# Kernel optimization log

Measured on AMD Instinct MI355X. Metric: run time of the kernel, lower is better.

## Reference

```python
import jax, jax.numpy as jnp
import numpy as np

BETA_MIN = 0.01
BETA_MAX = 0.995
EPS = 1e-6


def setup_inputs() -> dict:
    key = jax.random.key(0)
    k1, k2, k3, k4 = jax.random.split(key, 4)
    B, T, D = 16, 4096, 128
    return {
        "q": jax.random.normal(k1, (B, T, D), dtype=jnp.float32),
        "k": jax.random.normal(k2, (B, T, D), dtype=jnp.float32),
        "v": jax.random.normal(k3, (B, T, D), dtype=jnp.float32),
        "beta": jax.random.uniform(k4, (B, T, 1), dtype=jnp.float32),
        "mask": jnp.ones((B, T, 1), dtype=jnp.float32),
        "base_beta_1": jnp.asarray(2.0, dtype=jnp.float32),
        "base_beta_2": jnp.asarray(3.0, dtype=jnp.float32),
    }


def _delta_scan(q, k, v, beta, mask, base_beta_1, base_beta_2):
    B, T, D = q.shape
    phi_q = jax.nn.elu(q) + 1.0  # positive feature map
    phi_k = jax.nn.elu(k) + 1.0
    b1_base = jnp.clip(jax.nn.sigmoid(base_beta_1), BETA_MIN, BETA_MAX)
    b2_base = jnp.clip(jax.nn.sigmoid(base_beta_2), BETA_MIN, BETA_MAX)

    # time-major for scan: [T, B, ...]
    xs = (
        jnp.swapaxes(phi_q, 0, 1),
        jnp.swapaxes(phi_k, 0, 1),
        jnp.swapaxes(v, 0, 1),
        jnp.swapaxes(beta, 0, 1),
        jnp.swapaxes(mask, 0, 1),
    )

    H1 = jnp.zeros((B, D, D), dtype=q.dtype)
    H2 = jnp.zeros((B, D, D), dtype=q.dtype)
    Z1 = jnp.zeros((B, D), dtype=q.dtype)
    Z2 = jnp.zeros((B, D), dtype=q.dtype)

    def step(carry, x):
        H1, H2, Z1, Z2 = carry
        q_t, k_t, v_t, b_in_t, m_t = x  # q_t:[B,D], b_in_t/m_t:[B,1]
        b_in_t = jnp.clip(b_in_t, BETA_MIN, BETA_MAX)
        b1_t = jnp.clip(b1_base * b_in_t, BETA_MIN, BETA_MAX)  # [B,1]
        b2_t = jnp.clip(b2_base * b_in_t, BETA_MIN, BETA_MAX)
        kv = jnp.einsum('bd,be->bde', k_t, v_t) * m_t[:, :, None]  # masked outer product
        H1 = H1 * b1_t[:, :, None] + kv
        H2 = H2 * b2_t[:, :, None] + kv
        Z1 = Z1 * b1_t + k_t * m_t
        Z2 = Z2 * b2_t + k_t * m_t
        num = jnp.einsum('bd,bde->be', q_t, H1 + H2)
        den = jnp.maximum(jnp.sum(q_t * (Z1 + Z2), axis=-1, keepdims=True), EPS)
        o_t = num / den * m_t
        return (H1, H2, Z1, Z2), o_t

    _, outs = jax.lax.scan(step, (H1, H2, Z1, Z2), xs)
    return jnp.swapaxes(outs, 0, 1)  # [B, T, D]


def reference(q, k, v, beta, mask, base_beta_1, base_beta_2):
    return _delta_scan(q, k, v, beta, mask, base_beta_1, base_beta_2)
```

## Files before the change

### kernel.cpp

```cpp
#include <hip/hip_runtime.h>

#define B_ 16
#define T_ 4096
#define D_ 128
#define L_ 128
#define NC_ 32
#define CH_ (B_*NC_)
#define LDP 136

typedef __attribute__((ext_vector_type(8))) short bf16x8;
typedef __attribute__((ext_vector_type(4))) float f32x4;

__device__ __forceinline__ float clampf(float x, float lo, float hi) {
    return fminf(fmaxf(x, lo), hi);
}
__device__ __forceinline__ float phi_f(float x) {
    return x > 0.f ? x + 1.f : __expf(x);
}
__device__ __forceinline__ unsigned short bf16r(float f) {
    unsigned u = __builtin_bit_cast(unsigned, f);
    u += 0x7FFFu + ((u >> 16) & 1u);
    return (unsigned short)(u >> 16);
}
__device__ __forceinline__ float fbf(unsigned short h) {
    unsigned u = ((unsigned)h) << 16; return __builtin_bit_cast(float, u);
}
__device__ __forceinline__ unsigned pack2bf(float a, float b) {
    return (unsigned)bf16r(a) | ((unsigned)bf16r(b) << 16);
}
__device__ __forceinline__ uint4 pack8(const float* f) {
    uint4 r;
    r.x = pack2bf(f[0], f[1]); r.y = pack2bf(f[2], f[3]);
    r.z = pack2bf(f[4], f[5]); r.w = pack2bf(f[6], f[7]);
    return r;
}
__device__ __forceinline__ f32x4 zero4() { f32x4 z; z[0]=0.f; z[1]=0.f; z[2]=0.f; z[3]=0.f; return z; }

__device__ __forceinline__ int aidx(int row, int k0) {
    return (((row >> 4) * 4 + (k0 >> 5)) * 64 + ((k0 >> 3) & 3) * 16 + (row & 15)) * 8;
}

__global__ void k0w(const float* __restrict__ beta,
                    const float* __restrict__ bb1, const float* __restrict__ bb2,
                    float* __restrict__ lg1, float* __restrict__ lg2,
                    float* __restrict__ wexp) {
    int ch = blockIdx.x;
    int b = ch / NC_, c = ch % NC_;
    int tbase = b * T_ + c * L_;
    int tid = threadIdx.x;
    int lane = tid & 63, w = tid >> 6;
    __shared__ float tot1s[2], tot2s[2];

    float b1b = clampf(1.f / (1.f + __expf(-bb1[0])), 0.01f, 0.995f);
    float b2b = clampf(1.f / (1.f + __expf(-bb2[0])), 0.01f, 0.995f);
    float be = clampf(beta[tbase + tid], 0.01f, 0.995f);
    float x1 = __logf(clampf(b1b * be, 0.01f, 0.995f));
    float x2 = __logf(clampf(b2b * be, 0.01f, 0.995f));
#pragma unroll
    for (int off = 1; off < 64; off <<= 1) {
        float y1 = __shfl_up(x1, off);
        float y2 = __shfl_up(x2, off);
        if (lane >= off) { x1 += y1; x2 += y2; }
    }
    if (lane == 63) { tot1s[w] = x1; tot2s[w] = x2; }
    __syncthreads();
    if (w == 1) { x1 += tot1s[0]; x2 += tot2s[0]; }
    float tot1 = tot1s[0] + tot1s[1];
    float tot2 = tot2s[0] + tot2s[1];
    lg1[tbase + tid] = x1;
    lg2[tbase + tid] = x2;
    wexp[(size_t)ch * 128 + tid]                     = __expf(tot1 - x1);
    wexp[(size_t)CH_ * 128 + (size_t)ch * 128 + tid] = __expf(tot2 - x2);
}

__global__ __launch_bounds__(256) void kS(
        const float* __restrict__ kk, const float* __restrict__ vv,
        const float* __restrict__ mask,
        unsigned short* __restrict__ phiKT, unsigned short* __restrict__ VtT) {
    int g = blockIdx.x;
    int ch = g >> 2, q = g & 3;
    int b = ch / NC_, c = ch % NC_;
    int tbase = b * T_ + c * L_;
    int tid = threadIdx.x;
    size_t cb = (size_t)ch * 16384;

#pragma unroll
    for (int p = 0; p < 2; ++p) {
        int i = p * 256 + tid;
        int s = q * 32 + (i >> 4), d0 = (i & 15) * 8;
        const float* kp = &kk[(size_t)(tbase + s) * D_ + d0];
        float4 x0 = *(const float4*)kp, x1 = *(const float4*)(kp + 4);
        float m = mask[tbase + s];
        float pq[8] = {phi_f(x0.x)*m, phi_f(x0.y)*m, phi_f(x0.z)*m, phi_f(x0.w)*m,
                       phi_f(x1.x)*m, phi_f(x1.y)*m, phi_f(x1.z)*m, phi_f(x1.w)*m};
        *(uint4*)&phiKT[cb + aidx(s, d0)] = pack8(pq);
    }

#pragma unroll
    for (int p = 0; p < 2; ++p) {
        int i = p * 256 + tid;
        int e = q * 32 + (i & 31), s0 = (i >> 5) * 8;
        const float* vp = &vv[(size_t)(tbase + s0) * D_ + e];
        float f[8];
#pragma unroll
        for (int j = 0; j < 8; ++j)
            f[j] = vp[(size_t)j * D_];
        *(uint4*)&VtT[cb + aidx(e, s0)] = pack8(f);
    }
}

__global__ __launch_bounds__(512, 4) void kC(
        const float* __restrict__ kk, const float* __restrict__ mask,
        const unsigned short* __restrict__ VtT, const float* __restrict__ wexp,
        unsigned short* __restrict__ Cws, float* __restrict__ zc) {
    int g = blockIdx.x;
    int ch = ((g >> 4) << 3) | (g & 7);
    int st = (g >> 3) & 1;
    int b = ch / NC_, c = ch % NC_;
    int tbase = b * T_ + c * L_;
    int tid = threadIdx.x, lane = tid & 63, w = tid >> 6;
    int l15 = lane & 15, lg4 = lane >> 4;
    size_t cb = (size_t)ch * 16384;
    __shared__ unsigned short sKt[16384];

#pragma unroll
    for (int p = 0; p < 4; ++p) {
        int i = p * 512 + tid;
        int d = i & 127, s0 = (i >> 7) * 8;
        const float* kp = &kk[(size_t)(tbase + s0) * D_ + d];
        const float* mp = &mask[tbase + s0];
        float f[8];
#pragma unroll
        for (int j = 0; j < 8; ++j)
            f[j] = phi_f(kp[(size_t)j * D_]) * mp[j];
        *(uint4*)&sKt[aidx(d, s0)] = pack8(f);
    }
    __syncthreads();

    const float* wp = &wexp[(size_t)st * CH_ * 128 + (size_t)ch * 128];

    f32x4 acc[8];
#pragma unroll
    for (int n = 0; n < 8; ++n) acc[n] = zero4();
    float zp[8] = {0.f, 0.f, 0.f, 0.f, 0.f, 0.f, 0.f, 0.f};

#pragma unroll
    for (int ks = 0; ks < 4; ++ks) {
        int koff = ks * 32 + lg4 * 8;
        float wl[8];
        {
            float4 a0 = *(const float4*)&wp[koff];
            float4 a1 = *(const float4*)&wp[koff + 4];
            wl[0]=a0.x; wl[1]=a0.y; wl[2]=a0.z; wl[3]=a0.w;
            wl[4]=a1.x; wl[5]=a1.y; wl[6]=a1.z; wl[7]=a1.w;
        }
        bf16x8 as;
        {
            bf16x8 vt = *(const bf16x8*)&VtT[cb + (size_t)(((w * 4 + ks) * 64 + lane) * 8)];
#pragma unroll
            for (int j = 0; j < 8; ++j)
                as[j] = (short)bf16r(fbf((unsigned short)vt[j]) * wl[j]);
        }
        bf16x8 bb[8];
#pragma unroll
        for (int n = 0; n < 8; ++n)
            bb[n] = *(const bf16x8*)&sKt[((n * 4 + ks) * 64 + lane) * 8];
        if (w == 0) {
#pragma unroll
            for (int n = 0; n < 8; ++n)
#pragma unroll
                for (int j = 0; j < 8; ++j)
                    zp[n] += wl[j] * fbf((unsigned short)bb[n][j]);
        }
#pragma unroll
        for (int n = 0; n < 8; ++n)
            acc[n] = __builtin_amdgcn_mfma_f32_16x16x32_bf16(as, bb[n], acc[n], 0, 0, 0);
    }

    if (w == 0) {
#pragma unroll
        for (int n = 0; n < 8; ++n) {
            float z = zp[n];
            z += __shfl_xor(z, 16); z += __shfl_xor(z, 32);
            if (lg4 == 0)
                zc[((size_t)(st * B_ + b) * NC_ + c) * D_ + n * 16 + l15] = z;
        }
    }

    __syncthreads();
#pragma unroll
    for (int n = 0; n < 8; ++n)
#pragma unroll
        for (int r = 0; r < 4; ++r) {
            int e = w * 16 + lg4 * 4 + r;
            int d = n * 16 + l15;
            sKt[aidx(e, d & ~7) + (d & 7)] = bf16r(acc[n][r]);
        }
    __syncthreads();
    unsigned short* Cp = Cws + ((size_t)(st * B_ + b) * NC_ + c) * (D_ * D_);
#pragma unroll
    for (int p = 0; p < 4; ++p) {
        int i = p * 512 + tid;
        *(uint4*)&Cp[(size_t)i * 8] = *(const uint4*)&sKt[i * 8];
    }
}

__global__ void k2f(unsigned short* __restrict__ Cws, float* __restrict__ zc,
                    const float* __restrict__ lg1, const float* __restrict__ lg2) {
    int g = blockIdx.x * blockDim.x + threadIdx.x;
    if (g < 131072) {
        int st = g >> 16;
        int rem = g & 65535;
        int b = rem >> 12;
        int de = (rem & 4095) * 4;
        const float* lg = st ? lg2 : lg1;
        size_t base = ((size_t)(st * B_ + b) * NC_) * (D_ * D_) + de;
        float run0 = 0.f, run1 = 0.f, run2 = 0.f, run3 = 0.f;
#pragma unroll
        for (int c = 0; c < NC_; c++) {
            float a = __expf(lg[b * T_ + c * L_ + L_ - 1]);
            uint2 val = *(uint2*)&Cws[base + (size_t)c * (D_ * D_)];
            float t0 = fbf((unsigned short)(val.x & 0xffff)), t1 = fbf((unsigned short)(val.x >> 16));
            float t2 = fbf((unsigned short)(val.y & 0xffff)), t3 = fbf((unsigned short)(val.y >> 16));
            uint2 wv; wv.x = pack2bf(run0, run1); wv.y = pack2bf(run2, run3);
            *(uint2*)&Cws[base + (size_t)c * (D_ * D_)] = wv;
            run0 = a * run0 + t0; run1 = a * run1 + t1;
            run2 = a * run2 + t2; run3 = a * run3 + t3;
        }
    } else {
        int gz = g - 131072;
        int st = gz >> 11;
        int rem = gz & 2047;
        int b = rem >> 7;
        int d = rem & 127;
        const float* lg = st ? lg2 : lg1;
        size_t base = ((size_t)(st * B_ + b) * NC_) * D_ + d;
        float run = 0.f;
#pragma unroll
        for (int c = 0; c < NC_; c++) {
            float a = __expf(lg[b * T_ + c * L_ + L_ - 1]);
            float tmp = zc[base + (size_t)c * D_];
            zc[base + (size_t)c * D_] = run;
            run = a * run + tmp;
        }
    }
}

__global__ __launch_bounds__(512, 4) void k3_v7(
        const float* __restrict__ qq, const float* __restrict__ mask,
        const float* __restrict__ lg1, const float* __restrict__ lg2,
        const unsigned short* __restrict__ phiKT, const unsigned short* __restrict__ VtT,
        const unsigned short* __restrict__ Cws, const float* __restrict__ zc,
        float* __restrict__ out) {
    __shared__ unsigned short bufP[8][16 * LDP];
    int ch = blockIdx.x;
    int b = ch / NC_, c = ch % NC_;
    int tbase = b * T_ + c * L_;
    int tid = threadIdx.x, lane = tid & 63, w = tid >> 6;
    int l15 = lane & 15, lg4 = lane >> 4;
    unsigned short* bufPw = &bufP[w][0];
    size_t cb = (size_t)ch * 16384;

    int trow = w * 16 + l15;
    size_t gt = (size_t)(tbase + trow);

    float lg1t = lg1[gt], lg2t = lg2[gt], mt = mask[gt];
    float a1t = __expf(lg1t), a2t = __expf(lg2t);

    bf16x8 qf[4];
#pragma unroll
    for (int ks = 0; ks < 4; ++ks) {
        int koff = ks * 32 + lg4 * 8;
        const float* qp = &qq[gt * D_ + koff];
        float4 x0 = *(const float4*)qp, x1 = *(const float4*)(qp + 4);
        float p0[8] = {phi_f(x0.x), phi_f(x0.y), phi_f(x0.z), phi_f(x0.w),
                       phi_f(x1.x), phi_f(x1.y), phi_f(x1.z), phi_f(x1.w)};
#pragma unroll
        for (int j = 0; j < 8; ++j) qf[ks][j] = (short)bf16r(p0[j]);
    }

    const float* z1p = &zc[((size_t)(0 * B_ + b) * NC_ + c) * D_];
    const float* z2p = &zc[((size_t)(1 * B_ + b) * NC_ + c) * D_];
    float d1 = 0.f, d2 = 0.f;
#pragma unroll
    for (int ks = 0; ks < 4; ++ks) {
        int off = ks * 32 + lg4 * 8;
        float4 za = *(const float4*)(z1p + off), zb = *(const float4*)(z1p + off + 4);
        float4 zca = *(const float4*)(z2p + off), zcb = *(const float4*)(z2p + off + 4);
        float z1a[8] = {za.x, za.y, za.z, za.w, zb.x, zb.y, zb.z, zb.w};
        float z2a[8] = {zca.x, zca.y, zca.z, zca.w, zcb.x, zcb.y, zcb.z, zcb.w};
#pragma unroll
        for (int j = 0; j < 8; ++j) {
            float fq = fbf((unsigned short)qf[ks][j]);
            d1 += fq * z1a[j]; d2 += fq * z2a[j];
        }
    }
    d1 += __shfl_xor(d1, 16); d1 += __shfl_xor(d1, 32);
    d2 += __shfl_xor(d2, 16); d2 += __shfl_xor(d2, 32);

    int SN = (w | 1) + 1;
    int KP = SN >> 1;
    float rs = 0.f;
    for (int sp = 0; sp < KP; ++sp) {
        bf16x8 kf[8];
#pragma unroll
        for (int mm = 0; mm < 2; ++mm)
#pragma unroll
            for (int ks = 0; ks < 4; ++ks)
                kf[mm * 4 + ks] = *(const bf16x8*)&phiKT[cb + (size_t)(((((sp * 2 + mm) * 4) + ks) * 64 + lane) * 8)];
        f32x4 accs[2];
        accs[0] = zero4(); accs[1] = zero4();
#pragma unroll
        for (int ks = 0; ks < 4; ++ks)
#pragma unroll
            for (int mm = 0; mm < 2; ++mm)
                accs[mm] = __builtin_amdgcn_mfma_f32_16x16x32_bf16(kf[mm * 4 + ks], qf[ks], accs[mm], 0, 0, 0);
#pragma unroll
        for (int mm = 0; mm < 2; ++mm) {
            int s0 = (sp * 2 + mm) * 16 + lg4 * 4;
            float4 l1s = *(const float4*)&lg1[tbase + s0];
            float4 l2s = *(const float4*)&lg2[tbase + s0];
            float l1a[4] = {l1s.x, l1s.y, l1s.z, l1s.w};
            float l2a[4] = {l2s.x, l2s.y, l2s.z, l2s.w};
            float pv[4];
#pragma unroll
            for (int r = 0; r < 4; ++r) {
                int s = s0 + r;
                float p = 0.f;
                if (s <= trow)
                    p = accs[mm][r] * (__expf(lg1t - l1a[r]) + __expf(lg2t - l2a[r]));
                pv[r] = p; rs += p;
            }
            uint2 dd; dd.x = pack2bf(pv[0], pv[1]); dd.y = pack2bf(pv[2], pv[3]);
            *(uint2*)&bufPw[l15 * LDP + s0] = dd;
        }
    }
    rs += __shfl_xor(rs, 16); rs += __shfl_xor(rs, 32);
    float osc = mt / fmaxf(a1t * d1 + a2t * d2 + rs, 1e-6f);

    f32x4 acc_o[8];
#pragma unroll
    for (int m = 0; m < 8; ++m) acc_o[m] = zero4();
#pragma unroll
    for (int st = 0; st < 2; ++st) {
        const unsigned short* Hp = Cws + ((size_t)(st * B_ + b) * NC_ + c) * (D_ * D_);
        float sc = st ? a2t : a1t;
#pragma unroll
        for (int ks = 0; ks < 4; ++ks) {
            bf16x8 hf[8];
#pragma unroll
            for (int m = 0; m < 8; ++m)
                hf[m] = *(const bf16x8*)&Hp[(size_t)(((m * 4 + ks) * 64 + lane) * 8)];
            bf16x8 qs;
#pragma unroll
            for (int j = 0; j < 8; ++j)
                qs[j] = (short)bf16r(fbf((unsigned short)qf[ks][j]) * sc);
#pragma unroll
            for (int m = 0; m < 8; ++m)
                acc_o[m] = __builtin_amdgcn_mfma_f32_16x16x32_bf16(hf[m], qs, acc_o[m], 0, 0, 0);
        }
    }

    for (int ks = 0; ks < KP; ++ks) {
        bf16x8 vf[8];
#pragma unroll
        for (int m = 0; m < 8; ++m)
            vf[m] = *(const bf16x8*)&VtT[cb + (size_t)(((m * 4 + ks) * 64 + lane) * 8)];
        bf16x8 pf = *(const bf16x8*)&bufPw[l15 * LDP + ks * 32 + lg4 * 8];
#pragma unroll
        for (int m = 0; m < 8; ++m)
            acc_o[m] = __builtin_amdgcn_mfma_f32_16x16x32_bf16(vf[m], pf, acc_o[m], 0, 0, 0);
    }

#pragma unroll
    for (int m = 0; m < 8; ++m) {
        float4 o;
        o.x = acc_o[m][0] * osc; o.y = acc_o[m][1] * osc;
        o.z = acc_o[m][2] * osc; o.w = acc_o[m][3] * osc;
        *(float4*)&out[gt * D_ + m * 16 + lg4 * 4] = o;
    }
}

extern "C" void kernel_launch(void* const* d_in, const int* in_sizes, int n_in,
                              void* d_out, int out_size, void* d_ws, size_t ws_size,
                              hipStream_t stream) {
    const float* q    = (const float*)d_in[0];
    const float* k    = (const float*)d_in[1];
    const float* v    = (const float*)d_in[2];
    const float* beta = (const float*)d_in[3];
    const float* mask = (const float*)d_in[4];
    const float* bb1  = (const float*)d_in[5];
    const float* bb2  = (const float*)d_in[6];
    float* out = (float*)d_out;

    size_t n_lg = (size_t)B_ * T_;
    size_t n_z  = (size_t)2 * B_ * NC_ * D_;
    size_t n_w  = (size_t)2 * CH_ * 128;
    size_t n_C  = (size_t)2 * B_ * NC_ * D_ * D_;
    size_t n_kt = (size_t)B_ * T_ * D_;
    size_t need = (2 * n_lg + n_z + n_w) * sizeof(float) + (n_C + 2 * n_kt) * sizeof(unsigned short);
    if (ws_size < need) return;

    float* lg1  = (float*)d_ws;
    float* lg2  = lg1 + n_lg;
    float* zc   = lg2 + n_lg;
    float* wexp = zc + n_z;
    unsigned short* Cws    = (unsigned short*)(wexp + n_w);
    unsigned short* phiKT  = Cws + n_C;
    unsigned short* VtT    = phiKT + n_kt;

    k0w<<<CH_, 128, 0, stream>>>(beta, bb1, bb2, lg1, lg2, wexp);
    kS<<<4 * CH_, 256, 0, stream>>>(k, v, mask, phiKT, VtT);
    kC<<<2 * CH_, 512, 0, stream>>>(k, mask, VtT, wexp, Cws, zc);
    k2f<<<528, 256, 0, stream>>>(Cws, zc, lg1, lg2);
    k3_v7<<<CH_, 512, 0, stream>>>(q, mask, lg1, lg2, phiKT, VtT, Cws, zc, out);
}
```

Baseline: 91.77 us.

## Fuse decay prefix kernel into kS and restructure output stage by column tiles

Merges the per-chunk log-decay prefix-sum kernel into the phi(K)/V transpose kernel, dropping one launch. In the final kernel, each wave now owns one 16-wide output column tile across all 128 timesteps instead of one 16-row time tile. phi(Q), the output scales and the decay factors are staged in shared memory so that each wave loads only its own slice of the chunk states and V rather than the full matrices. This trades fewer global loads of the state matrices for a block barrier, extra LDS traffic, an fp32 rescale of the state contribution instead of a bf16 one, and launch bounds lowered from 4 to 2 blocks per CU.

```diff
diff --git a/kernel.cpp b/kernel.cpp
--- a/kernel.cpp
+++ b/kernel.cpp
@@ -40,49 +40,47 @@
     return (((row >> 4) * 4 + (k0 >> 5)) * 64 + ((k0 >> 3) & 3) * 16 + (row & 15)) * 8;
 }
 
-__global__ void k0w(const float* __restrict__ beta,
-                    const float* __restrict__ bb1, const float* __restrict__ bb2,
-                    float* __restrict__ lg1, float* __restrict__ lg2,
-                    float* __restrict__ wexp) {
-    int ch = blockIdx.x;
-    int b = ch / NC_, c = ch % NC_;
-    int tbase = b * T_ + c * L_;
-    int tid = threadIdx.x;
-    int lane = tid & 63, w = tid >> 6;
-    __shared__ float tot1s[2], tot2s[2];
-
-    float b1b = clampf(1.f / (1.f + __expf(-bb1[0])), 0.01f, 0.995f);
-    float b2b = clampf(1.f / (1.f + __expf(-bb2[0])), 0.01f, 0.995f);
-    float be = clampf(beta[tbase + tid], 0.01f, 0.995f);
-    float x1 = __logf(clampf(b1b * be, 0.01f, 0.995f));
-    float x2 = __logf(clampf(b2b * be, 0.01f, 0.995f));
-#pragma unroll
-    for (int off = 1; off < 64; off <<= 1) {
-        float y1 = __shfl_up(x1, off);
-        float y2 = __shfl_up(x2, off);
-        if (lane >= off) { x1 += y1; x2 += y2; }
-    }
-    if (lane == 63) { tot1s[w] = x1; tot2s[w] = x2; }
-    __syncthreads();
-    if (w == 1) { x1 += tot1s[0]; x2 += tot2s[0]; }
-    float tot1 = tot1s[0] + tot1s[1];
-    float tot2 = tot2s[0] + tot2s[1];
-    lg1[tbase + tid] = x1;
-    lg2[tbase + tid] = x2;
-    wexp[(size_t)ch * 128 + tid]                     = __expf(tot1 - x1);
-    wexp[(size_t)CH_ * 128 + (size_t)ch * 128 + tid] = __expf(tot2 - x2);
-}
-
 __global__ __launch_bounds__(256) void kS(
         const float* __restrict__ kk, const float* __restrict__ vv,
         const float* __restrict__ mask,
-        unsigned short* __restrict__ phiKT, unsigned short* __restrict__ VtT) {
+        const float* __restrict__ beta,
+        const float* __restrict__ bb1, const float* __restrict__ bb2,
+        unsigned short* __restrict__ phiKT, unsigned short* __restrict__ VtT,
+        float* __restrict__ lg1, float* __restrict__ lg2, float* __restrict__ wexp) {
     int g = blockIdx.x;
     int ch = g >> 2, q = g & 3;
     int b = ch / NC_, c = ch % NC_;
     int tbase = b * T_ + c * L_;
     int tid = threadIdx.x;
     size_t cb = (size_t)ch * 16384;
+    __shared__ float tot1s[2], tot2s[2];
+
+    float cx1 = 0.f, cx2 = 0.f;
+    int clane = tid & 63, cw = tid >> 6;
+    if (q == 0 && tid < 128) {
+        float b1b = clampf(1.f / (1.f + __expf(-bb1[0])), 0.01f, 0.995f);
+        float b2b = clampf(1.f / (1.f + __expf(-bb2[0])), 0.01f, 0.995f);
+        float be = clampf(beta[tbase + tid], 0.01f, 0.995f);
+        cx1 = __logf(clampf(b1b * be, 0.01f, 0.995f));
+        cx2 = __logf(clampf(b2b * be, 0.01f, 0.995f));
+#pragma unroll
+        for (int off = 1; off < 64; off <<= 1) {
+            float y1 = __shfl_up(cx1, off);
+            float y2 = __shfl_up(cx2, off);
+            if (clane >= off) { cx1 += y1; cx2 += y2; }
+        }
+        if (clane == 63) { tot1s[cw] = cx1; tot2s[cw] = cx2; }
+    }
+    __syncthreads();
+    if (q == 0 && tid < 128) {
+        if (cw == 1) { cx1 += tot1s[0]; cx2 += tot2s[0]; }
+        float tot1 = tot1s[0] + tot1s[1];
+        float tot2 = tot2s[0] + tot2s[1];
+        lg1[tbase + tid] = cx1;
+        lg2[tbase + tid] = cx2;
+        wexp[(size_t)ch * 128 + tid]                     = __expf(tot1 - cx1);
+        wexp[(size_t)CH_ * 128 + (size_t)ch * 128 + tid] = __expf(tot2 - cx2);
+    }
 
 #pragma unroll
     for (int p = 0; p < 2; ++p) {
@@ -246,138 +244,163 @@
     }
 }
 
-__global__ __launch_bounds__(512, 4) void k3_v7(
+__global__ __launch_bounds__(512, 2) void k3_v9(
         const float* __restrict__ qq, const float* __restrict__ mask,
         const float* __restrict__ lg1, const float* __restrict__ lg2,
         const unsigned short* __restrict__ phiKT, const unsigned short* __restrict__ VtT,
         const unsigned short* __restrict__ Cws, const float* __restrict__ zc,
         float* __restrict__ out) {
+    __shared__ unsigned short sQ[128 * LDP];
     __shared__ unsigned short bufP[8][16 * LDP];
+    __shared__ float sOsc[128], sA1[128], sA2[128];
     int ch = blockIdx.x;
     int b = ch / NC_, c = ch % NC_;
     int tbase = b * T_ + c * L_;
     int tid = threadIdx.x, lane = tid & 63, w = tid >> 6;
     int l15 = lane & 15, lg4 = lane >> 4;
-    unsigned short* bufPw = &bufP[w][0];
     size_t cb = (size_t)ch * 16384;
 
-    int trow = w * 16 + l15;
-    size_t gt = (size_t)(tbase + trow);
-
-    float lg1t = lg1[gt], lg2t = lg2[gt], mt = mask[gt];
-    float a1t = __expf(lg1t), a2t = __expf(lg2t);
-
-    bf16x8 qf[4];
-#pragma unroll
-    for (int ks = 0; ks < 4; ++ks) {
-        int koff = ks * 32 + lg4 * 8;
-        const float* qp = &qq[gt * D_ + koff];
-        float4 x0 = *(const float4*)qp, x1 = *(const float4*)(qp + 4);
-        float p0[8] = {phi_f(x0.x), phi_f(x0.y), phi_f(x0.z), phi_f(x0.w),
-                       phi_f(x1.x), phi_f(x1.y), phi_f(x1.z), phi_f(x1.w)};
-#pragma unroll
-        for (int j = 0; j < 8; ++j) qf[ks][j] = (short)bf16r(p0[j]);
-    }
-
-    const float* z1p = &zc[((size_t)(0 * B_ + b) * NC_ + c) * D_];
-    const float* z2p = &zc[((size_t)(1 * B_ + b) * NC_ + c) * D_];
-    float d1 = 0.f, d2 = 0.f;
-#pragma unroll
-    for (int ks = 0; ks < 4; ++ks) {
-        int off = ks * 32 + lg4 * 8;
-        float4 za = *(const float4*)(z1p + off), zb = *(const float4*)(z1p + off + 4);
-        float4 zca = *(const float4*)(z2p + off), zcb = *(const float4*)(z2p + off + 4);
-        float z1a[8] = {za.x, za.y, za.z, za.w, zb.x, zb.y, zb.z, zb.w};
-        float z2a[8] = {zca.x, zca.y, zca.z, zca.w, zcb.x, zcb.y, zcb.z, zcb.w};
-#pragma unroll
-        for (int j = 0; j < 8; ++j) {
-            float fq = fbf((unsigned short)qf[ks][j]);
-            d1 += fq * z1a[j]; d2 += fq * z2a[j];
-        }
-    }
-    d1 += __shfl_xor(d1, 16); d1 += __shfl_xor(d1, 32);
-    d2 += __shfl_xor(d2, 16); d2 += __shfl_xor(d2, 32);
-
-    int SN = (w | 1) + 1;
-    int KP = SN >> 1;
-    float rs = 0.f;
-    for (int sp = 0; sp < KP; ++sp) {
-        bf16x8 kf[8];
-#pragma unroll
-        for (int mm = 0; mm < 2; ++mm)
+    {
+        int trow = w * 16 + l15;
+        size_t gt = (size_t)(tbase + trow);
+        float lg1t = lg1[gt], lg2t = lg2[gt], mt = mask[gt];
+        float a1t = __expf(lg1t), a2t = __expf(lg2t);
+
+        bf16x8 qf[4];
+#pragma unroll
+        for (int ks = 0; ks < 4; ++ks) {
+            int koff = ks * 32 + lg4 * 8;
+            const float* qp = &qq[gt * D_ + koff];
+            float4 x0 = *(const float4*)qp, x1 = *(const float4*)(qp + 4);
+            float p0[8] = {phi_f(x0.x), phi_f(x0.y), phi_f(x0.z), phi_f(x0.w),
+                           phi_f(x1.x), phi_f(x1.y), phi_f(x1.z), phi_f(x1.w)};
+#pragma unroll
+            for (int j = 0; j < 8; ++j) qf[ks][j] = (short)bf16r(p0[j]);
+            *(uint4*)&sQ[trow * LDP + koff] = __builtin_bit_cast(uint4, qf[ks]);
+        }
+
+        const float* z1p = &zc[((size_t)(0 * B_ + b) * NC_ + c) * D_];
+        const float* z2p = &zc[((size_t)(1 * B_ + b) * NC_ + c) * D_];
+        float d1 = 0.f, d2 = 0.f;
+#pragma unroll
+        for (int ks = 0; ks < 4; ++ks) {
+            int off = ks * 32 + lg4 * 8;
+            float4 za = *(const float4*)(z1p + off), zb = *(const float4*)(z1p + off + 4);
+            float4 zca = *(const float4*)(z2p + off), zcb = *(const float4*)(z2p + off + 4);
+            float z1a[8] = {za.x, za.y, za.z, za.w, zb.x, zb.y, zb.z, zb.w};
+            float z2a[8] = {zca.x, zca.y, zca.z, zca.w, zcb.x, zcb.y, zcb.z, zcb.w};
+#pragma unroll
+            for (int j = 0; j < 8; ++j) {
+                float fq = fbf((unsigned short)qf[ks][j]);
+                d1 += fq * z1a[j]; d2 += fq * z2a[j];
+            }
+        }
+        d1 += __shfl_xor(d1, 16); d1 += __shfl_xor(d1, 32);
+        d2 += __shfl_xor(d2, 16); d2 += __shfl_xor(d2, 32);
+
+        int SN = (w | 1) + 1;
+        int KP = SN >> 1;
+        float rs = 0.f;
+        for (int sp = 0; sp < KP; ++sp) {
+            bf16x8 kf[8];
+#pragma unroll
+            for (int mm = 0; mm < 2; ++mm)
+#pragma unroll
+                for (int ks = 0; ks < 4; ++ks)
+                    kf[mm * 4 + ks] = *(const bf16x8*)&phiKT[cb + (size_t)(((((sp * 2 + mm) * 4) + ks) * 64 + lane) * 8)];
+            f32x4 accs[2];
+            accs[0] = zero4(); accs[1] = zero4();
 #pragma unroll
             for (int ks = 0; ks < 4; ++ks)
-                kf[mm * 4 + ks] = *(const bf16x8*)&phiKT[cb + (size_t)(((((sp * 2 + mm) * 4) + ks) * 64 + lane) * 8)];
-        f32x4 accs[2];
-        accs[0] = zero4(); accs[1] = zero4();
+#pragma unroll
+                for (int mm = 0; mm < 2; ++mm)
+                    accs[mm] = __builtin_amdgcn_mfma_f32_16x16x32_bf16(kf[mm * 4 + ks], qf[ks], accs[mm], 0, 0, 0);
+#pragma unroll
+            for (int mm = 0; mm < 2; ++mm) {
+                int s0 = (sp * 2 + mm) * 16 + lg4 * 4;
+                float4 l1s = *(const float4*)&lg1[tbase + s0];
+                float4 l2s = *(const float4*)&lg2[tbase + s0];
+                float l1a[4] = {l1s.x, l1s.y, l1s.z, l1s.w};
+                float l2a[4] = {l2s.x, l2s.y, l2s.z, l2s.w};
+                float pv[4];
+#pragma unroll
+                for (int r = 0; r < 4; ++r) {
+                    int s = s0 + r;
+                    float p = 0.f;
+                    if (s <= trow)
+                        p = accs[mm][r] * (__expf(lg1t - l1a[r]) + __expf(lg2t - l2a[r]));
+                    pv[r] = p; rs += p;
+                }
+                uint2 dd; dd.x = pack2bf(pv[0], pv[1]); dd.y = pack2bf(pv[2], pv[3]);
+                *(uint2*)&bufP[w][l15 * LDP + s0] = dd;
+            }
+        }
+        rs += __shfl_xor(rs, 16); rs += __shfl_xor(rs, 32);
+        float osc = mt / fmaxf(a1t * d1 + a2t * d2 + rs, 1e-6f);
+        if (lg4 == 0) {
+            sOsc[trow] = osc;
+            sA1[trow] = a1t;
+            sA2[trow] = a2t;
+        }
+    }
+    __syncthreads();
+
+    {
+        int m = w;
+        bf16x8 vf[4];
 #pragma unroll
         for (int ks = 0; ks < 4; ++ks)
-#pragma unroll
-            for (int mm = 0; mm < 2; ++mm)
-                accs[mm] = __builtin_amdgcn_mfma_f32_16x16x32_bf16(kf[mm * 4 + ks], qf[ks], accs[mm], 0, 0, 0);
-#pragma unroll
-        for (int mm = 0; mm < 2; ++mm) {
-            int s0 = (sp * 2 + mm) * 16 + lg4 * 4;
-            float4 l1s = *(const float4*)&lg1[tbase + s0];
-            float4 l2s = *(const float4*)&lg2[tbase + s0];
-            float l1a[4] = {l1s.x, l1s.y, l1s.z, l1s.w};
-            float l2a[4] = {l2s.x, l2s.y, l2s.z, l2s.w};
-            float pv[4];
-#pragma unroll
-            for (int r = 0; r < 4; ++r) {
-                int s = s0 + r;
-                float p = 0.f;
-                if (s <= trow)
-                    p = accs[mm][r] * (__expf(lg1t - l1a[r]) + __expf(lg2t - l2a[r]));
-                pv[r] = p; rs += p;
+            vf[ks] = *(const bf16x8*)&VtT[cb + (size_t)(((m * 4 + ks) * 64 + lane) * 8)];
+
+        f32x4 accO[8];
+#pragma unroll
+        for (int tt = 0; tt < 8; ++tt) accO[tt] = zero4();
+
+#pragma unroll
+        for (int st = 0; st < 2; ++st) {
+            const unsigned short* Hp = Cws + ((size_t)(st * B_ + b) * NC_ + c) * (D_ * D_);
+            bf16x8 hf[4];
+#pragma unroll
+            for (int ks = 0; ks < 4; ++ks)
+                hf[ks] = *(const bf16x8*)&Hp[(size_t)(((m * 4 + ks) * 64 + lane) * 8)];
+            f32x4 U[8];
+#pragma unroll
+            for (int tt = 0; tt < 8; ++tt) U[tt] = zero4();
+#pragma unroll
+            for (int ks = 0; ks < 4; ++ks) {
+                int koff = ks * 32 + lg4 * 8;
+#pragma unroll
+                for (int tt = 0; tt < 8; ++tt) {
+                    bf16x8 qb = *(const bf16x8*)&sQ[(tt * 16 + l15) * LDP + koff];
+                    U[tt] = __builtin_amdgcn_mfma_f32_16x16x32_bf16(hf[ks], qb, U[tt], 0, 0, 0);
+                }
             }
-            uint2 dd; dd.x = pack2bf(pv[0], pv[1]); dd.y = pack2bf(pv[2], pv[3]);
-            *(uint2*)&bufPw[l15 * LDP + s0] = dd;
-        }
-    }
-    rs += __shfl_xor(rs, 16); rs += __shfl_xor(rs, 32);
-    float osc = mt / fmaxf(a1t * d1 + a2t * d2 + rs, 1e-6f);
-
-    f32x4 acc_o[8];
-#pragma unroll
-    for (int m = 0; m < 8; ++m) acc_o[m] = zero4();
-#pragma unroll
-    for (int st = 0; st < 2; ++st) {
-        const unsigned short* Hp = Cws + ((size_t)(st * B_ + b) * NC_ + c) * (D_ * D_);
-        float sc = st ? a2t : a1t;
-#pragma unroll
-        for (int ks = 0; ks < 4; ++ks) {
-            bf16x8 hf[8];
-#pragma unroll
-            for (int m = 0; m < 8; ++m)
-                hf[m] = *(const bf16x8*)&Hp[(size_t)(((m * 4 + ks) * 64 + lane) * 8)];
-            bf16x8 qs;
-#pragma unroll
-            for (int j = 0; j < 8; ++j)
-                qs[j] = (short)bf16r(fbf((unsigned short)qf[ks][j]) * sc);
-#pragma unroll
-            for (int m = 0; m < 8; ++m)
-                acc_o[m] = __builtin_amdgcn_mfma_f32_16x16x32_bf16(hf[m], qs, acc_o[m], 0, 0, 0);
-        }
-    }
-
-    for (int ks = 0; ks < KP; ++ks) {
-        bf16x8 vf[8];
-#pragma unroll
-        for (int m = 0; m < 8; ++m)
-            vf[m] = *(const bf16x8*)&VtT[cb + (size_t)(((m * 4 + ks) * 64 + lane) * 8)];
-        bf16x8 pf = *(const bf16x8*)&bufPw[l15 * LDP + ks * 32 + lg4 * 8];
-#pragma unroll
-        for (int m = 0; m < 8; ++m)
-            acc_o[m] = __builtin_amdgcn_mfma_f32_16x16x32_bf16(vf[m], pf, acc_o[m], 0, 0, 0);
-    }
-
-#pragma unroll
-    for (int m = 0; m < 8; ++m) {
-        float4 o;
-        o.x = acc_o[m][0] * osc; o.y = acc_o[m][1] * osc;
-        o.z = acc_o[m][2] * osc; o.w = acc_o[m][3] * osc;
-        *(float4*)&out[gt * D_ + m * 16 + lg4 * 4] = o;
+            const float* sA = st ? sA2 : sA1;
+#pragma unroll
+            for (int tt = 0; tt < 8; ++tt) {
+                float sc = sA[tt * 16 + l15];
+#pragma unroll
+                for (int r = 0; r < 4; ++r) accO[tt][r] += sc * U[tt][r];
+            }
+        }
+
+#pragma unroll
+        for (int tt = 0; tt < 8; ++tt) {
+            int KP = ((tt | 1) + 1) >> 1;
+            for (int ks = 0; ks < KP; ++ks) {
+                bf16x8 pf = *(const bf16x8*)&bufP[tt][l15 * LDP + ks * 32 + lg4 * 8];
+                accO[tt] = __builtin_amdgcn_mfma_f32_16x16x32_bf16(vf[ks], pf, accO[tt], 0, 0, 0);
+            }
+        }
+
+#pragma unroll
+        for (int tt = 0; tt < 8; ++tt) {
+            float osc = sOsc[tt * 16 + l15];
+            float4 o;
+            o.x = accO[tt][0] * osc; o.y = accO[tt][1] * osc;
+            o.z = accO[tt][2] * osc; o.w = accO[tt][3] * osc;
+            *(float4*)&out[(size_t)(tbase + tt * 16 + l15) * D_ + m * 16 + lg4 * 4] = o;
+        }
     }
 }
 
@@ -409,9 +432,8 @@
     unsigned short* phiKT  = Cws + n_C;
     unsigned short* VtT    = phiKT + n_kt;
 
-    k0w<<<CH_, 128, 0, stream>>>(beta, bb1, bb2, lg1, lg2, wexp);
-    kS<<<4 * CH_, 256, 0, stream>>>(k, v, mask, phiKT, VtT);
+    kS<<<4 * CH_, 256, 0, stream>>>(k, v, mask, beta, bb1, bb2, phiKT, VtT, lg1, lg2, wexp);
     kC<<<2 * CH_, 512, 0, stream>>>(k, mask, VtT, wexp, Cws, zc);
     k2f<<<528, 256, 0, stream>>>(Cws, zc, lg1, lg2);
-    k3_v7<<<CH_, 512, 0, stream>>>(q, mask, lg1, lg2, phiKT, VtT, Cws, zc, out);
-}
+    k3_v9<<<CH_, 512, 0, stream>>>(q, mask, lg1, lg2, phiKT, VtT, Cws, zc, out);
+}
```

After: 78.45 us. 14.5% less time.
